# Performance work log

Measured on AMD Instinct MI355X. Metric: run time of the kernel, lower is better.

## Reference

```python
import jax, jax.numpy as jnp
import numpy as np
import math

D, H, F = 1024, 16, 4096
DH = D // H
EPS_LN = 1e-5


def _layernorm(x, scale, bias):
    mu = jnp.mean(x, axis=-1, keepdims=True)
    var = jnp.mean(jnp.square(x - mu), axis=-1, keepdims=True)
    return (x - mu) * jax.lax.rsqrt(var + EPS_LN) * scale + bias


def setup_inputs() -> dict:
    key = jax.random.key(0)
    ks = jax.random.split(key, 16)
    B, T = 2, 2048
    src = jax.random.normal(ks[0], (B, T, D), dtype=jnp.float32)
    attn_mask = jax.random.randint(ks[1], (T, T), 0, 2) == 1  # bool [T,S], True = masked
    xavier = lambda k, shp: jax.random.uniform(k, shp, jnp.float32, -1.0, 1.0) * math.sqrt(6.0 / (shp[0] + shp[1]))
    return {
        "src": src, "attn_mask": attn_mask,
        "q_w": xavier(ks[2], (D, D)), "q_b": jnp.zeros((D,), jnp.float32),
        "k_w": xavier(ks[3], (D, D)), "k_b": jnp.zeros((D,), jnp.float32),
        "v_w": xavier(ks[4], (D, D)), "v_b": jnp.zeros((D,), jnp.float32),
        "o_w": xavier(ks[5], (D, D)), "o_b": jnp.zeros((D,), jnp.float32),
        "l1_w": xavier(ks[6], (F, D)), "l1_b": jnp.zeros((F,), jnp.float32),
        "l2_w": xavier(ks[7], (D, F)), "l2_b": jnp.zeros((D,), jnp.float32),
        "n1_s": jnp.ones((D,), jnp.float32), "n1_b": jnp.zeros((D,), jnp.float32),
        "n2_s": jnp.ones((D,), jnp.float32), "n2_b": jnp.zeros((D,), jnp.float32),
        "alpha_attn": jax.random.normal(ks[8], (), jnp.float32) * 0.1,
        "alpha_ff": jax.random.normal(ks[9], (), jnp.float32) * 0.1,
    }


def reference(src, attn_mask, q_w, q_b, k_w, k_b, v_w, v_b, o_w, o_b,
              l1_w, l1_b, l2_w, l2_b, n1_s, n1_b, n2_s, n2_b,
              alpha_attn, alpha_ff):
    B, T, _ = src.shape
    # --- self-attention block (post-norm layer, dropout=0 => identity) ---
    q = (src @ q_w.T + q_b).reshape(B, T, H, DH).transpose(0, 2, 1, 3)  # [B,H,T,DH]
    k = (src @ k_w.T + k_b).reshape(B, T, H, DH).transpose(0, 2, 1, 3)
    v = (src @ v_w.T + v_b).reshape(B, T, H, DH).transpose(0, 2, 1, 3)
    scores = jnp.einsum('bhtd,bhsd->bhts', q, k) / math.sqrt(DH)  # [B,H,T,S]
    scores = jnp.where(attn_mask[None, None, :, :], -jnp.inf, scores)
    probs = jax.nn.softmax(scores + 1e-9, axis=-1)
    probs = jnp.where(jnp.isinf(scores), 0.0, probs)  # zero where masked (custom semantics)
    attn = jnp.einsum('bhts,bhsd->bhtd', probs, v).transpose(0, 2, 1, 3).reshape(B, T, D)
    attn = attn @ o_w.T + o_b
    x = _layernorm(src + alpha_attn * attn, n1_s, n1_b)
    # --- FFN block ---
    ff = jax.nn.relu(x @ l1_w.T + l1_b) @ l2_w.T + l2_b
    x = _layernorm(x + alpha_ff * ff, n2_s, n2_b)
    return x
```

## Files before the change

### kernel.cpp

```cpp
#include <hip/hip_runtime.h>
#include <math.h>

#define Dm 1024
#define Hh 16
#define DHd 64
#define Ff 4096
#define Tt 2048
#define Bb 2

#define ATT_C2 0.18033688011112042f

typedef __bf16 bf16_8 __attribute__((ext_vector_type(8)));
typedef __bf16 bf16x2 __attribute__((ext_vector_type(2)));
typedef __bf16 bf16x4 __attribute__((ext_vector_type(4)));
typedef float  f32x4  __attribute__((ext_vector_type(4)));
typedef float  f32x16 __attribute__((ext_vector_type(16)));
typedef unsigned int u32x4 __attribute__((ext_vector_type(4)));
typedef unsigned int u32x8s __attribute__((ext_vector_type(8)));

__device__ __forceinline__ unsigned short f2bf(float f) {
    unsigned int u = __float_as_uint(f);
    unsigned int r = (u + 0x7fffu + ((u >> 16) & 1u)) >> 16;
    return (unsigned short)r;
}

__device__ __forceinline__ bf16x2 pkbf(float a, float b) {
#if __has_builtin(__builtin_amdgcn_cvt_pk_bf16_f32)
    return __builtin_amdgcn_cvt_pk_bf16_f32(a, b);
#else
    bf16x2 r; r[0] = (__bf16)a; r[1] = (__bf16)b; return r;
#endif
}
__device__ __forceinline__ bf16x4 pkbf4(float a, float b, float c, float d) {
    bf16x2 lo = pkbf(a, b), hi = pkbf(c, d);
    return __builtin_shufflevector(lo, hi, 0, 1, 2, 3);
}

__device__ __forceinline__ void plswap32(unsigned &a, unsigned &b) {
#if __has_builtin(__builtin_amdgcn_permlane32_swap)
    auto r = __builtin_amdgcn_permlane32_swap((int)a, (int)b, false, false);
    a = (unsigned)r[0]; b = (unsigned)r[1];
#else
    asm volatile("v_permlane32_swap_b32 %0, %1" : "+v"(a), "+v"(b));
#endif
}

__device__ __forceinline__ void gld_lds16(const void* g, void* l) {
    __builtin_amdgcn_global_load_lds(
        (const __attribute__((address_space(1))) void*)g,
        (__attribute__((address_space(3))) void*)l,
        16, 0, 0);
}

__device__ __forceinline__ void sload32(const unsigned* p,
        u32x8s &a, u32x8s &b, u32x8s &c, u32x8s &d) {
    asm volatile(
        "s_load_dwordx8 %0, %4, 0x0\n\t"
        "s_load_dwordx8 %1, %4, 0x20\n\t"
        "s_load_dwordx8 %2, %4, 0x40\n\t"
        "s_load_dwordx8 %3, %4, 0x60\n\t"
        "s_waitcnt lgkmcnt(0)"
        : "=&s"(a), "=&s"(b), "=&s"(c), "=&s"(d)
        : "s"(p));
}

__device__ __forceinline__ float selkeep(float e, unsigned long long keep) {
    float r;
    asm("v_cndmask_b32 %0, 0, %1, %2" : "=v"(r) : "v"(e), "s"(keep));
    return r;
}

__global__ __launch_bounds__(256) void preprocess_kernel(
    const float* __restrict__ q_w, const float* __restrict__ k_w,
    const float* __restrict__ v_w, const float* __restrict__ o_w,
    const float* __restrict__ l1_w, const float* __restrict__ l2_w,
    const float* __restrict__ src, const int* __restrict__ mask,
    const float* __restrict__ q_b, const float* __restrict__ k_b,
    unsigned short* __restrict__ qkw, unsigned short* __restrict__ vw16,
    unsigned short* __restrict__ ow,  unsigned short* __restrict__ l1w,
    unsigned short* __restrict__ l2w, unsigned short* __restrict__ srcb,
    unsigned* __restrict__ mbT, float* __restrict__ qkb)
{
    const int bid = blockIdx.x;
    const int tid = threadIdx.x;
    if (bid < 16384) {
        int i = bid * 256 + tid;
        const float* sp; unsigned short* dp; int off;
        if (i < 1048576) {
            if (i < 262144)      { sp = q_w; dp = qkw;           off = i; }
            else if (i < 524288) { sp = k_w; dp = qkw + 1048576; off = i - 262144; }
            else if (i < 786432) { sp = v_w; dp = vw16;          off = i - 524288; }
            else                 { sp = o_w; dp = ow;            off = i - 786432; }
        } else if (i < 2097152)  { sp = l1_w; dp = l1w;          off = i - 1048576; }
        else if (i < 3145728)    { sp = l2_w; dp = l2w;          off = i - 2097152; }
        else                     { sp = src;  dp = srcb;         off = i - 3145728; }
        float4 v = ((const float4*)sp)[off];
        ((bf16x4*)dp)[off] = pkbf4(v.x, v.y, v.z, v.w);
    } else if (bid < 16896) {
        int w = (bid - 16384) * 256 + tid;
        int tw32 = w >> 11, s = w & 2047;
        const int* p = mask + (size_t)(tw32 * 32) * 2048 + s;
        unsigned bits = 0;
        #pragma unroll
        for (int j = 0; j < 32; ++j)
            bits |= (p[(size_t)j * 2048] == 0 ? 1u : 0u) << j;
        mbT[w] = bits;
    } else {
        int i = (bid - 16896) * 256 + tid;
        qkb[i] = (i < 1024) ? q_b[i] : k_b[i - 1024];
    }
}

template<int RELU, int BF16OUT>
__global__ __launch_bounds__(256) void gemm_bf16_kernel(
    const unsigned short* __restrict__ A, const unsigned short* __restrict__ W,
    const float* __restrict__ bias, void* __restrict__ C, void* __restrict__ C2,
    int M, int N, int K, int ldc, int ksub)
{
    __shared__ __bf16 As[128][64];
    __shared__ __bf16 Bs[128][64];
    const int tid  = threadIdx.x;
    const int lane = tid & 63;
    const int wave = tid >> 6;
    const int m0 = blockIdx.y * 128;
    const int n0 = blockIdx.x * 128;
    const int lr8 = lane >> 3;
    const int gch = (lane & 7) ^ lr8;
    const int wm = (wave & 1) * 64;
    const int wn = (wave >> 1) * 64;
    const int quad = lane >> 4;
    const int lm = lane & 15;
    const int z  = blockIdx.z;
    const int kstart = z * ksub;
    void* Cz = (z == 0) ? C : C2;

    f32x4 acc[4][4];
    #pragma unroll
    for (int i = 0; i < 4; i++)
        #pragma unroll
        for (int j = 0; j < 4; j++) {
            acc[i][j][0] = 0.f; acc[i][j][1] = 0.f;
            acc[i][j][2] = 0.f; acc[i][j][3] = 0.f;
        }

    for (int k0 = kstart; k0 < kstart + ksub; k0 += 64) {
        __syncthreads();
        #pragma unroll
        for (int i = 0; i < 4; i++) {
            int seg = wave * 4 + i;
            int r = seg * 8 + lr8;
            gld_lds16(A + (size_t)(m0 + r) * K + k0 + gch * 8, &As[seg * 8][0]);
            gld_lds16(W + (size_t)(n0 + r) * K + k0 + gch * 8, &Bs[seg * 8][0]);
        }
        __syncthreads();
        #pragma unroll
        for (int kh = 0; kh < 2; kh++) {
            bf16_8 af[4], bfr[4];
            #pragma unroll
            for (int t = 0; t < 4; t++) {
                int ch = (kh * 4 + quad) ^ (lm & 7);
                af[t]  = *(const bf16_8*)&As[wm + t * 16 + lm][ch * 8];
                bfr[t] = *(const bf16_8*)&Bs[wn + t * 16 + lm][ch * 8];
            }
            #pragma unroll
            for (int i = 0; i < 4; i++)
                #pragma unroll
                for (int j = 0; j < 4; j++)
                    acc[i][j] = __builtin_amdgcn_mfma_f32_16x16x32_bf16(
                        af[i], bfr[j], acc[i][j], 0, 0, 0);
        }
    }

    float bvc[4];
    #pragma unroll
    for (int j = 0; j < 4; j++)
        bvc[j] = (z == 0) ? bias[n0 + wn + j * 16 + lm] : 0.f;

    #pragma unroll
    for (int i = 0; i < 4; i++)
        #pragma unroll
        for (int j = 0; j < 4; j++) {
            int col = n0 + wn + j * 16 + lm;
            #pragma unroll
            for (int r = 0; r < 4; r++) {
                int row = m0 + wm + i * 16 + quad * 4 + r;
                float v = acc[i][j][r] + bvc[j];
                if (RELU) v = fmaxf(v, 0.f);
                if (BF16OUT)
                    ((unsigned short*)Cz)[(size_t)row * ldc + col] = f2bf(v);
                else
                    ((float*)Cz)[(size_t)row * ldc + col] = v;
            }
        }
}

__global__ __launch_bounds__(256, 2) void gemm_ffn1_kernel(
    const unsigned short* __restrict__ A, const unsigned short* __restrict__ W,
    const float* __restrict__ bias, unsigned short* __restrict__ C)
{
    __shared__ __bf16 As[256][64];
    __shared__ __bf16 Bs[128][64];
    const int tid  = threadIdx.x;
    const int lane = tid & 63;
    const int wave = tid >> 6;
    const int m0 = blockIdx.y * 256;
    const int n0 = blockIdx.x * 128;
    const int lr8 = lane >> 3;
    const int gch = (lane & 7) ^ lr8;
    const int quad = lane >> 4;
    const int lm = lane & 15;

    f32x4 acc[4][8];
    #pragma unroll
    for (int i = 0; i < 4; i++)
        #pragma unroll
        for (int j = 0; j < 8; j++) {
            acc[i][j][0] = 0.f; acc[i][j][1] = 0.f;
            acc[i][j][2] = 0.f; acc[i][j][3] = 0.f;
        }

    for (int k0 = 0; k0 < 1024; k0 += 64) {
        __syncthreads();
        #pragma unroll
        for (int i = 0; i < 8; i++) {
            int seg = wave * 8 + i;
            int r = seg * 8 + lr8;
            gld_lds16(A + (size_t)(m0 + r) * 1024 + k0 + gch * 8, &As[seg * 8][0]);
        }
        #pragma unroll
        for (int i = 0; i < 4; i++) {
            int seg = wave * 4 + i;
            int r = seg * 8 + lr8;
            gld_lds16(W + (size_t)(n0 + r) * 1024 + k0 + gch * 8, &Bs[seg * 8][0]);
        }
        __syncthreads();
        #pragma unroll
        for (int kh = 0; kh < 2; kh++) {
            const int ch = (kh * 4 + quad) ^ (lm & 7);
            bf16_8 af[4], bfr[8];
            #pragma unroll
            for (int t = 0; t < 4; t++)
                af[t] = *(const bf16_8*)&As[wave * 64 + t * 16 + lm][ch * 8];
            #pragma unroll
            for (int j = 0; j < 8; j++)
                bfr[j] = *(const bf16_8*)&Bs[j * 16 + lm][ch * 8];
            #pragma unroll
            for (int i = 0; i < 4; i++)
                #pragma unroll
                for (int j = 0; j < 8; j++)
                    acc[i][j] = __builtin_amdgcn_mfma_f32_16x16x32_bf16(
                        af[i], bfr[j], acc[i][j], 0, 0, 0);
        }
    }

    float bv[8];
    #pragma unroll
    for (int j = 0; j < 8; j++) bv[j] = bias[n0 + j * 16 + lm];

    #pragma unroll
    for (int i = 0; i < 4; i++)
        #pragma unroll
        for (int j = 0; j < 8; j++) {
            int col = n0 + j * 16 + lm;
            #pragma unroll
            for (int r = 0; r < 4; r++) {
                int row = m0 + wave * 64 + i * 16 + quad * 4 + r;
                float v = fmaxf(acc[i][j][r] + bv[j], 0.f);
                C[(size_t)row * Ff + col] = f2bf(v);
            }
        }
}

__global__ __launch_bounds__(256) void gemm_qkvt_kernel(
    const unsigned short* __restrict__ srcb, const unsigned short* __restrict__ qkw,
    const unsigned short* __restrict__ vw16, const float* __restrict__ qkb,
    const float* __restrict__ v_b,
    unsigned short* __restrict__ qk16, unsigned short* __restrict__ vtf)
{
    const int bid = blockIdx.x;
    const unsigned short *A, *W;
    const float* bias;
    unsigned short* C;
    int m0, n0, ldc;
    bool qscale, rowbias;
    if (bid < 512) {
        A = srcb; W = qkw; bias = qkb; C = qk16;
        n0 = (bid & 15) * 128; m0 = (bid >> 4) * 128;
        ldc = 2048; qscale = true; rowbias = false;
    } else {
        int b2 = bid - 512;
        A = vw16; W = srcb; bias = v_b; C = vtf;
        n0 = (b2 & 31) * 128; m0 = (b2 >> 5) * 128;
        ldc = 4096; qscale = false; rowbias = true;
    }
    const int K = 1024;

    __shared__ __bf16 As[128][64];
    __shared__ __bf16 Bs[128][64];
    const int tid  = threadIdx.x;
    const int lane = tid & 63;
    const int wave = tid >> 6;
    const int lr8 = lane >> 3;
    const int gch = (lane & 7) ^ lr8;
    const int wm = (wave & 1) * 64;
    const int wn = (wave >> 1) * 64;
    const int quad = lane >> 4;
    const int lm = lane & 15;

    f32x4 acc[4][4];
    #pragma unroll
    for (int i = 0; i < 4; i++)
        #pragma unroll
        for (int j = 0; j < 4; j++) {
            acc[i][j][0] = 0.f; acc[i][j][1] = 0.f;
            acc[i][j][2] = 0.f; acc[i][j][3] = 0.f;
        }

    for (int k0 = 0; k0 < K; k0 += 64) {
        __syncthreads();
        #pragma unroll
        for (int i = 0; i < 4; i++) {
            int seg = wave * 4 + i;
            int r = seg * 8 + lr8;
            gld_lds16(A + (size_t)(m0 + r) * K + k0 + gch * 8, &As[seg * 8][0]);
            gld_lds16(W + (size_t)(n0 + r) * K + k0 + gch * 8, &Bs[seg * 8][0]);
        }
        __syncthreads();
        #pragma unroll
        for (int kh = 0; kh < 2; kh++) {
            bf16_8 af[4], bfr[4];
            #pragma unroll
            for (int t = 0; t < 4; t++) {
                int ch = (kh * 4 + quad) ^ (lm & 7);
                af[t]  = *(const bf16_8*)&As[wm + t * 16 + lm][ch * 8];
                bfr[t] = *(const bf16_8*)&Bs[wn + t * 16 + lm][ch * 8];
            }
            #pragma unroll
            for (int i = 0; i < 4; i++)
                #pragma unroll
                for (int j = 0; j < 4; j++)
                    acc[i][j] = __builtin_amdgcn_mfma_f32_16x16x32_bf16(
                        af[i], bfr[j], acc[i][j], 0, 0, 0);
        }
    }

    float bvc[4];
    float brr[4][4];
    if (!rowbias) {
        #pragma unroll
        for (int j = 0; j < 4; j++) bvc[j] = bias[n0 + wn + j * 16 + lm];
    } else {
        #pragma unroll
        for (int i = 0; i < 4; i++) {
            float4 t4 = *(const float4*)&bias[m0 + wm + i * 16 + quad * 4];
            brr[i][0] = t4.x; brr[i][1] = t4.y; brr[i][2] = t4.z; brr[i][3] = t4.w;
        }
    }

    #pragma unroll
    for (int i = 0; i < 4; i++)
        #pragma unroll
        for (int j = 0; j < 4; j++) {
            int col = n0 + wn + j * 16 + lm;
            #pragma unroll
            for (int r = 0; r < 4; r++) {
                int row = m0 + wm + i * 16 + quad * 4 + r;
                float v = acc[i][j][r] + (rowbias ? brr[i][r] : bvc[j]);
                if (qscale && col < 1024) v *= ATT_C2;
                C[(size_t)row * ldc + col] = f2bf(v);
            }
        }
}

__global__ __launch_bounds__(512, 4) void attn_mfma_kernel(
    const unsigned short* __restrict__ qk,
    const unsigned short* __restrict__ vt,
    const unsigned* __restrict__ mbT,
    unsigned short* __restrict__ out)
{
    __shared__ __align__(16) char smem[65536];
    __bf16* KsP = (__bf16*)smem;
    __bf16* VtP = (__bf16*)(smem + 32768);

    const int tid  = threadIdx.x;
    const int lane = tid & 63;
    const int wave = tid >> 6;
    const int l31  = lane & 31;
    const int hi   = lane >> 5;
    const int x7   = l31 & 7;
    const int bh = blockIdx.y;
    const int b = bh >> 4, h = bh & 15;
    const int wvu = __builtin_amdgcn_readfirstlane(wave);
    const int wq  = wvu & 3;
    const int sh  = wvu >> 2;
    const int tw = blockIdx.x * 128 + wq * 32;
    const unsigned* mrow = mbT + (size_t)(blockIdx.x * 4 + wq) * 2048;

    bf16_8 qf[4];
    #pragma unroll
    for (int ds4 = 0; ds4 < 4; ++ds4)
        qf[ds4] = *(const bf16_8*)(qk +
            (size_t)(b * Tt + tw + l31) * 2048 + h * DHd + ds4 * 16 + hi * 8);

    f32x16 oacc[2];
    f32x16 ol;
    f32x16 z16;
    #pragma unroll
    for (int r = 0; r < 16; ++r) {
        oacc[0][r] = 0.f; oacc[1][r] = 0.f; ol[r] = 0.f; z16[r] = 0.f;
    }
    bf16_8 vone;
    {
        __bf16 one = (__bf16)1.0f;
        #pragma unroll
        for (int j = 0; j < 8; ++j) vone[j] = one;
    }

    const int krow8 = lane >> 3;
    const int kj    = (lane & 7) ^ krow8;
    const int vr4   = lane >> 4;

    auto STAGE = [&](int nb, int s0) {
        #pragma unroll
        for (int i = 0; i < 2; ++i) {
            int ci = wave * 2 + i;
            {
                int r = 8 * ci + krow8;
                const unsigned short* g = qk +
                    (size_t)(b * Tt + s0 + r) * 2048 + 1024 + h * DHd + kj * 8;
                gld_lds16(g, &KsP[nb * 8192 + ci * 512]);
            }
            {
                int d = 4 * ci + vr4;
                int jj = (lane & 15) ^ (d & 7);
                const unsigned short* g = vt +
                    (size_t)(h * DHd + d) * 4096 + b * Tt + s0 + jj * 8;
                gld_lds16(g, &VtP[nb * 8192 + ci * 512]);
            }
        }
    };

    STAGE(0, 0);

    for (int st = 0; st < 16; ++st) {
        const int cb = st & 1;
        const int s0 = st * 128;
        __syncthreads();

        if (st < 15) STAGE(cb ^ 1, s0 + 128);

        #pragma unroll
        for (int sbl = 0; sbl < 2; ++sbl) {
            const int sb = sh * 2 + sbl;
            u32x8s ma, mbw, mc, md;
            sload32(mrow + s0 + sb * 32, ma, mbw, mc, md);

            f32x16 sacc = z16;
            #pragma unroll
            for (int ds4 = 0; ds4 < 4; ++ds4) {
                bf16_8 kf = *(const bf16_8*)&KsP[cb * 8192 +
                    (sb * 32 + l31) * 64 + (((ds4 * 2 + hi) ^ x7) * 8)];
                sacc = __builtin_amdgcn_mfma_f32_32x32x16_bf16(
                    kf, qf[ds4], sacc, 0, 0, 0);
            }
            float p[16];
            #pragma unroll
            for (int g = 0; g < 4; ++g) {
                u32x8s vv = (g == 0) ? ma : (g == 1) ? mbw : (g == 2) ? mc : md;
                #pragma unroll
                for (int m = 0; m < 4; ++m) {
                    const int reg = g * 4 + m;
                    unsigned long long keep =
                        ((unsigned long long)vv[m + 4] << 32) |
                        (unsigned long long)vv[m];
                    float e = __builtin_amdgcn_exp2f(sacc[reg]);
                    p[reg] = selkeep(e, keep);
                }
            }
            unsigned u[4], v[4];
            #pragma unroll
            for (int g = 0; g < 4; ++g) {
                u[g] = __builtin_bit_cast(unsigned, pkbf(p[g * 4 + 0], p[g * 4 + 1]));
                v[g] = __builtin_bit_cast(unsigned, pkbf(p[g * 4 + 2], p[g * 4 + 3]));
            }
            plswap32(u[0], u[1]); plswap32(v[0], v[1]);
            plswap32(u[2], u[3]); plswap32(v[2], v[3]);
            u32x4 w0; w0[0] = u[0]; w0[1] = v[0]; w0[2] = u[1]; w0[3] = v[1];
            u32x4 w1; w1[0] = u[2]; w1[1] = v[2]; w1[2] = u[3]; w1[3] = v[3];
            bf16_8 pa0 = __builtin_bit_cast(bf16_8, w0);
            bf16_8 pa1 = __builtin_bit_cast(bf16_8, w1);
            #pragma unroll
            for (int kst = 0; kst < 2; ++kst) {
                bf16_8 pa = kst ? pa1 : pa0;
                #pragma unroll
                for (int dblk = 0; dblk < 2; ++dblk) {
                    int cpos = (sb * 4 + kst * 2 + hi) ^ x7;
                    bf16_8 vf = *(const bf16_8*)&VtP[cb * 8192 +
                        ((dblk * 32 + l31) * 16 + cpos) * 8];
                    oacc[dblk] = __builtin_amdgcn_mfma_f32_32x32x16_bf16(
                        pa, vf, oacc[dblk], 0, 0, 0);
                }
                ol = __builtin_amdgcn_mfma_f32_32x32x16_bf16(
                    pa, vone, ol, 0, 0, 0);
            }
        }
    }

    __syncthreads();
    float* comb = (float*)smem;
    if (sh == 1) {
        #pragma unroll
        for (int dblk = 0; dblk < 2; ++dblk)
            #pragma unroll
            for (int q = 0; q < 4; ++q) {
                float4 v4 = { oacc[dblk][q * 4 + 0], oacc[dblk][q * 4 + 1],
                              oacc[dblk][q * 4 + 2], oacc[dblk][q * 4 + 3] };
                *(float4*)&comb[wq * 3072 + (dblk * 4 + q) * 256 + lane * 4] = v4;
            }
        #pragma unroll
        for (int q = 0; q < 4; ++q) {
            float4 v4 = { ol[q * 4 + 0], ol[q * 4 + 1],
                          ol[q * 4 + 2], ol[q * 4 + 3] };
            *(float4*)&comb[wq * 3072 + (8 + q) * 256 + lane * 4] = v4;
        }
    }
    __syncthreads();
    if (sh == 0) {
        #pragma unroll
        for (int dblk = 0; dblk < 2; ++dblk)
            #pragma unroll
            for (int q = 0; q < 4; ++q) {
                float4 v4 = *(const float4*)&comb[
                    wq * 3072 + (dblk * 4 + q) * 256 + lane * 4];
                oacc[dblk][q * 4 + 0] += v4.x; oacc[dblk][q * 4 + 1] += v4.y;
                oacc[dblk][q * 4 + 2] += v4.z; oacc[dblk][q * 4 + 3] += v4.w;
            }
        #pragma unroll
        for (int q = 0; q < 4; ++q) {
            float4 v4 = *(const float4*)&comb[
                wq * 3072 + (8 + q) * 256 + lane * 4];
            ol[q * 4 + 0] += v4.x; ol[q * 4 + 1] += v4.y;
            ol[q * 4 + 2] += v4.z; ol[q * 4 + 3] += v4.w;
        }
        #pragma unroll
        for (int g = 0; g < 4; ++g)
            #pragma unroll
            for (int m = 0; m < 4; ++m) {
                const int reg = g * 4 + m;
                const int tr = m + 8 * g + 4 * hi;
                float l = ol[reg];
                float inv = (l > 0.f) ? 1.f / l : 0.f;
                int row = b * Tt + tw + tr;
                #pragma unroll
                for (int dblk = 0; dblk < 2; ++dblk)
                    out[(size_t)row * Dm + h * DHd + dblk * 32 + l31] =
                        f2bf(oacc[dblk][reg] * inv);
            }
    }
}

template<int NPARTS, int BASEBF, int OUTF32, int OUTBF>
__global__ __launch_bounds__(256) void residual_ln_kernel(
    const void* __restrict__ base, const float* __restrict__ d0,
    const float* __restrict__ d1,
    const float* __restrict__ alpha_p, const float* __restrict__ scale,
    const float* __restrict__ bias, float* __restrict__ out,
    unsigned short* __restrict__ out_bf)
{
    const int row = blockIdx.x;
    const int tid = threadIdx.x;
    const float alpha = alpha_p[0];
    float4 xb;
    if (BASEBF) {
        bf16x4 bb = ((const bf16x4*)((const unsigned short*)base + (size_t)row * Dm))[tid];
        xb.x = (float)bb[0]; xb.y = (float)bb[1]; xb.z = (float)bb[2]; xb.w = (float)bb[3];
    } else {
        xb = ((const float4*)((const float*)base + (size_t)row * Dm))[tid];
    }
    float4 xd = ((const float4*)(d0 + (size_t)row * Dm))[tid];
    if (NPARTS == 2) {
        float4 x2 = ((const float4*)(d1 + (size_t)row * Dm))[tid];
        xd.x += x2.x; xd.y += x2.y; xd.z += x2.z; xd.w += x2.w;
    }
    float4 x;
    x.x = xb.x + alpha * xd.x;
    x.y = xb.y + alpha * xd.y;
    x.z = xb.z + alpha * xd.z;
    x.w = xb.w + alpha * xd.w;
    float s  = x.x + x.y + x.z + x.w;
    float sq = x.x*x.x + x.y*x.y + x.z*x.z + x.w*x.w;
    #pragma unroll
    for (int off = 32; off > 0; off >>= 1) {
        s  += __shfl_down(s, off, 64);
        sq += __shfl_down(sq, off, 64);
    }
    __shared__ float red[8];
    const int w = tid >> 6;
    if ((tid & 63) == 0) { red[w] = s; red[4 + w] = sq; }
    __syncthreads();
    s  = red[0] + red[1] + red[2] + red[3];
    sq = red[4] + red[5] + red[6] + red[7];
    const float mu  = s * (1.f / Dm);
    const float var = sq * (1.f / Dm) - mu * mu;
    const float r   = rsqrtf(var + 1e-5f);
    float4 sc = ((const float4*)scale)[tid];
    float4 bi = ((const float4*)bias)[tid];
    float4 o;
    o.x = (x.x - mu) * r * sc.x + bi.x;
    o.y = (x.y - mu) * r * sc.y + bi.y;
    o.z = (x.z - mu) * r * sc.z + bi.z;
    o.w = (x.w - mu) * r * sc.w + bi.w;
    if (OUTF32)
        ((float4*)(out + (size_t)row * Dm))[tid] = o;
    if (OUTBF)
        ((bf16x4*)(out_bf + (size_t)row * Dm))[tid] = pkbf4(o.x, o.y, o.z, o.w);
}

extern "C" void kernel_launch(void* const* d_in, const int* in_sizes, int n_in,
                              void* d_out, int out_size, void* d_ws, size_t ws_size,
                              hipStream_t stream)
{
    (void)in_sizes; (void)n_in; (void)out_size; (void)ws_size;
    const float* src  = (const float*)d_in[0];
    const int*   mask = (const int*)  d_in[1];
    const float* q_w  = (const float*)d_in[2];
    const float* q_b  = (const float*)d_in[3];
    const float* k_w  = (const float*)d_in[4];
    const float* k_b  = (const float*)d_in[5];
    const float* v_w  = (const float*)d_in[6];
    const float* v_b  = (const float*)d_in[7];
    const float* o_w  = (const float*)d_in[8];
    const float* o_b  = (const float*)d_in[9];
    const float* l1_w = (const float*)d_in[10];
    const float* l1_b = (const float*)d_in[11];
    const float* l2_w = (const float*)d_in[12];
    const float* l2_b = (const float*)d_in[13];
    const float* n1_s = (const float*)d_in[14];
    const float* n1_b = (const float*)d_in[15];
    const float* n2_s = (const float*)d_in[16];
    const float* n2_b = (const float*)d_in[17];
    const float* a_attn = (const float*)d_in[18];
    const float* a_ff   = (const float*)d_in[19];

    const size_t MB = 1024 * 1024;
    char* w = (char*)d_ws;
    unsigned short* qkw  = (unsigned short*)(w + 0);
    unsigned short* vw16 = (unsigned short*)(w + 4  * MB);
    unsigned short* ow   = (unsigned short*)(w + 6  * MB);
    unsigned short* l1w  = (unsigned short*)(w + 8  * MB);
    unsigned short* l2w  = (unsigned short*)(w + 16 * MB);
    unsigned short* srcb = (unsigned short*)(w + 24 * MB);
    unsigned short* qk16 = (unsigned short*)(w + 32 * MB);
    unsigned short* vtf  = (unsigned short*)(w + 48 * MB);
    unsigned*       mbT  = (unsigned*)      (w + 56 * MB);
    float*          qkb  = (float*)         (w + 56 * MB + 524288);
    unsigned short* atb  = (unsigned short*)(w + 24 * MB);
    float*          o0   = (float*)         (w + 58 * MB);
    float*          o1   = (float*)         (w + 74 * MB);
    unsigned short* x1b  = (unsigned short*)(w + 48 * MB);
    unsigned short* hb   = (unsigned short*)(w + 58 * MB);
    float*          fp0  = (float*)         (w + 0);
    float*          fp1  = (float*)         (w + 32 * MB);

    const int MR = Bb * Tt;
    dim3 blk(256);

    preprocess_kernel<<<dim3(16904), blk, 0, stream>>>(
        q_w, k_w, v_w, o_w, l1_w, l2_w, src, mask, q_b, k_b,
        qkw, vw16, ow, l1w, l2w, srcb, mbT, qkb);
    gemm_qkvt_kernel<<<dim3(768), blk, 0, stream>>>(
        srcb, qkw, vw16, qkb, v_b, qk16, vtf);
    attn_mfma_kernel<<<dim3(16, 32), dim3(512), 0, stream>>>(qk16, vtf, mbT, atb);
    gemm_bf16_kernel<0, 0><<<dim3(8, 32, 2), blk, 0, stream>>>(
        atb, ow, o_b, o0, o1, MR, Dm, Dm, Dm, 512);
    residual_ln_kernel<2, 0, 0, 1><<<dim3(MR), blk, 0, stream>>>(
        src, o0, o1, a_attn, n1_s, n1_b, nullptr, x1b);
    gemm_ffn1_kernel<<<dim3(32, 16), blk, 0, stream>>>(x1b, l1w, l1_b, hb);
    gemm_bf16_kernel<0, 0><<<dim3(8, 32, 2), blk, 0, stream>>>(
        hb, l2w, l2_b, fp0, fp1, MR, Dm, Ff, Dm, Ff / 2);
    residual_ln_kernel<2, 1, 1, 0><<<dim3(MR), blk, 0, stream>>>(
        x1b, fp0, fp1, a_ff, n2_s, n2_b, (float*)d_out, nullptr);
}
```

Measured before the change: 356.3 us.

## Use 8-wave intra-block split-K GEMM for out-proj and FFN2 with LDS reduction

Replaces the 4-wave 128x128 GEMM with a 512-thread kernel that loads a 128-wide K slice per iteration. Each half of the waves handles one 64-wide K half on the same output tile, and the two partial sums are combined through LDS before the epilogue. This halves the number of loop iterations and barriers per tile and doubles the waves available to hide memory latency. In exchange it uses 64KB of LDS per block, which limits occupancy, and adds an LDS reduction step.

```diff
diff --git a/kernel.cpp b/kernel.cpp
--- a/kernel.cpp
+++ b/kernel.cpp
@@ -111,28 +111,33 @@
     }
 }
 
-template<int RELU, int BF16OUT>
-__global__ __launch_bounds__(256) void gemm_bf16_kernel(
+__global__ __launch_bounds__(512, 4) void gemm_splitk8_kernel(
     const unsigned short* __restrict__ A, const unsigned short* __restrict__ W,
-    const float* __restrict__ bias, void* __restrict__ C, void* __restrict__ C2,
-    int M, int N, int K, int ldc, int ksub)
+    const float* __restrict__ bias, float* __restrict__ C, float* __restrict__ C2,
+    int K, int ldc, int ksub)
 {
-    __shared__ __bf16 As[128][64];
-    __shared__ __bf16 Bs[128][64];
+    __shared__ __align__(16) char smem[65536];
+    __bf16* As = (__bf16*)smem;
+    __bf16* Bs = (__bf16*)(smem + 32768);
+
     const int tid  = threadIdx.x;
     const int lane = tid & 63;
     const int wave = tid >> 6;
+    const int wvu  = __builtin_amdgcn_readfirstlane(wave);
+    const int wq   = wvu & 3;
+    const int kh   = wvu >> 2;
     const int m0 = blockIdx.y * 128;
     const int n0 = blockIdx.x * 128;
-    const int lr8 = lane >> 3;
-    const int gch = (lane & 7) ^ lr8;
-    const int wm = (wave & 1) * 64;
-    const int wn = (wave >> 1) * 64;
+    const int wm = (wq & 1) * 64;
+    const int wn = (wq >> 1) * 64;
     const int quad = lane >> 4;
     const int lm = lane & 15;
     const int z  = blockIdx.z;
     const int kstart = z * ksub;
-    void* Cz = (z == 0) ? C : C2;
+    float* Cz = (z == 0) ? C : C2;
+
+    const int lr4 = lane >> 4;
+    const int lc  = lane & 15;
 
     f32x4 acc[4][4];
     #pragma unroll
@@ -143,24 +148,28 @@
             acc[i][j][2] = 0.f; acc[i][j][3] = 0.f;
         }
 
-    for (int k0 = kstart; k0 < kstart + ksub; k0 += 64) {
+    for (int k0 = kstart; k0 < kstart + ksub; k0 += 128) {
         __syncthreads();
         #pragma unroll
-        for (int i = 0; i < 4; i++) {
+        for (int i = 0; i < 4; ++i) {
             int seg = wave * 4 + i;
-            int r = seg * 8 + lr8;
-            gld_lds16(A + (size_t)(m0 + r) * K + k0 + gch * 8, &As[seg * 8][0]);
-            gld_lds16(W + (size_t)(n0 + r) * K + k0 + gch * 8, &Bs[seg * 8][0]);
+            int r = seg * 4 + lr4;
+            int ch = lc ^ (r & 7);
+            gld_lds16(A + (size_t)(m0 + r) * K + k0 + ch * 8, &As[seg * 512]);
+            gld_lds16(W + (size_t)(n0 + r) * K + k0 + ch * 8, &Bs[seg * 512]);
         }
         __syncthreads();
         #pragma unroll
-        for (int kh = 0; kh < 2; kh++) {
+        for (int kk = 0; kk < 2; ++kk) {
             bf16_8 af[4], bfr[4];
             #pragma unroll
-            for (int t = 0; t < 4; t++) {
-                int ch = (kh * 4 + quad) ^ (lm & 7);
-                af[t]  = *(const bf16_8*)&As[wm + t * 16 + lm][ch * 8];
-                bfr[t] = *(const bf16_8*)&Bs[wn + t * 16 + lm][ch * 8];
+            for (int t = 0; t < 4; ++t) {
+                int ra = wm + t * 16 + lm;
+                int ca = (kh * 8 + kk * 4 + quad) ^ (ra & 7);
+                af[t]  = *(const bf16_8*)&As[ra * 128 + ca * 8];
+                int rb = wn + t * 16 + lm;
+                int cb = (kh * 8 + kk * 4 + quad) ^ (rb & 7);
+                bfr[t] = *(const bf16_8*)&Bs[rb * 128 + cb * 8];
             }
             #pragma unroll
             for (int i = 0; i < 4; i++)
@@ -171,27 +180,36 @@
         }
     }
 
-    float bvc[4];
-    #pragma unroll
-    for (int j = 0; j < 4; j++)
-        bvc[j] = (z == 0) ? bias[n0 + wn + j * 16 + lm] : 0.f;
-
-    #pragma unroll
-    for (int i = 0; i < 4; i++)
-        #pragma unroll
-        for (int j = 0; j < 4; j++) {
-            int col = n0 + wn + j * 16 + lm;
-            #pragma unroll
-            for (int r = 0; r < 4; r++) {
-                int row = m0 + wm + i * 16 + quad * 4 + r;
-                float v = acc[i][j][r] + bvc[j];
-                if (RELU) v = fmaxf(v, 0.f);
-                if (BF16OUT)
-                    ((unsigned short*)Cz)[(size_t)row * ldc + col] = f2bf(v);
-                else
-                    ((float*)Cz)[(size_t)row * ldc + col] = v;
-            }
-        }
+    __syncthreads();
+    float* comb = (float*)smem;
+    if (kh == 1) {
+        #pragma unroll
+        for (int i = 0; i < 4; i++)
+            #pragma unroll
+            for (int j = 0; j < 4; j++)
+                *(f32x4*)&comb[wq * 4096 + (i * 4 + j) * 256 + lane * 4] =
+                    acc[i][j];
+    }
+    __syncthreads();
+    if (kh == 0) {
+        float bvc[4];
+        #pragma unroll
+        for (int j = 0; j < 4; j++)
+            bvc[j] = (z == 0) ? bias[n0 + wn + j * 16 + lm] : 0.f;
+        #pragma unroll
+        for (int i = 0; i < 4; i++)
+            #pragma unroll
+            for (int j = 0; j < 4; j++) {
+                f32x4 v4 = *(const f32x4*)&comb[
+                    wq * 4096 + (i * 4 + j) * 256 + lane * 4];
+                int col = n0 + wn + j * 16 + lm;
+                #pragma unroll
+                for (int r = 0; r < 4; r++) {
+                    int row = m0 + wm + i * 16 + quad * 4 + r;
+                    Cz[(size_t)row * ldc + col] = acc[i][j][r] + v4[r] + bvc[j];
+                }
+            }
+    }
 }
 
 __global__ __launch_bounds__(256, 2) void gemm_ffn1_kernel(
@@ -671,13 +689,13 @@
     gemm_qkvt_kernel<<<dim3(768), blk, 0, stream>>>(
         srcb, qkw, vw16, qkb, v_b, qk16, vtf);
     attn_mfma_kernel<<<dim3(16, 32), dim3(512), 0, stream>>>(qk16, vtf, mbT, atb);
-    gemm_bf16_kernel<0, 0><<<dim3(8, 32, 2), blk, 0, stream>>>(
-        atb, ow, o_b, o0, o1, MR, Dm, Dm, Dm, 512);
+    gemm_splitk8_kernel<<<dim3(8, 32, 2), dim3(512), 0, stream>>>(
+        atb, ow, o_b, o0, o1, Dm, Dm, 512);
     residual_ln_kernel<2, 0, 0, 1><<<dim3(MR), blk, 0, stream>>>(
         src, o0, o1, a_attn, n1_s, n1_b, nullptr, x1b);
     gemm_ffn1_kernel<<<dim3(32, 16), blk, 0, stream>>>(x1b, l1w, l1_b, hb);
-    gemm_bf16_kernel<0, 0><<<dim3(8, 32, 2), blk, 0, stream>>>(
-        hb, l2w, l2_b, fp0, fp1, MR, Dm, Ff, Dm, Ff / 2);
+    gemm_splitk8_kernel<<<dim3(8, 32, 2), dim3(512), 0, stream>>>(
+        hb, l2w, l2_b, fp0, fp1, Ff, Dm, 2048);
     residual_ln_kernel<2, 1, 1, 0><<<dim3(MR), blk, 0, stream>>>(
         x1b, fp0, fp1, a_ff, n2_s, n2_b, (float*)d_out, nullptr);
 }
```

Measured after the change: 356.2 us. No clear change (-0.1%).
